# Kernel optimization log

Measured on AMD Instinct MI355X. Metric: run time of the kernel, lower is better.

## Reference

```python
import jax, jax.numpy as jnp
import numpy as np

BN_EPS = 1e-5


def setup_inputs() -> dict:
    key = jax.random.key(0)
    k1, k2, k3 = jax.random.split(key, 3)
    N, C_in, T, V = 32, 64, 288, 25
    C_out = 64
    fv = jax.random.normal(k1, (N, C_in, T, V), dtype=jnp.float32)
    adj = jax.random.uniform(k2, (V, V), dtype=jnp.float32)
    # Conv2d(2*C_in, C_out, 1x1) weight flattened to [C_out, 2*C_in]; kaiming-ish scale
    W = jax.random.normal(k3, (C_out, 2 * C_in), dtype=jnp.float32) * (2.0 / (2 * C_in)) ** 0.5
    b = jnp.zeros((C_out,), dtype=jnp.float32)
    gamma = jnp.ones((C_out,), dtype=jnp.float32)   # bn_init scale=1
    beta = jnp.zeros((C_out,), dtype=jnp.float32)
    return {"fv": fv, "adj": adj, "W": W, "b": b, "gamma": gamma, "beta": beta}


def reference(fv, adj, W, b, gamma, beta):
    # fv: [N, C, T, V]; neighbor aggregation over joints via learnable adjacency
    fv_agg = jnp.einsum('nctv,vy->ncty', fv, adj)
    cat = jnp.concatenate([fv, fv_agg], axis=1)            # [N, 2C, T, V]
    # 1x1 conv == channel matmul
    out = jnp.einsum('ncty,oc->noty', cat, W) + b[None, :, None, None]
    # BatchNorm2d in training mode: batch stats over (N, T, V) per channel
    mean = out.mean(axis=(0, 2, 3), keepdims=True)
    var = out.var(axis=(0, 2, 3), keepdims=True)
    out = (out - mean) * jax.lax.rsqrt(var + BN_EPS)
    out = out * gamma[None, :, None, None] + beta[None, :, None, None]
    return jax.nn.relu(out)
```

## Files before the change

### kernel.cpp

```cpp
#include <hip/hip_runtime.h>

#define N_DIM 32
#define C_IN 64
#define C_OUT 64
#define T_DIM 288
#define V_DIM 25
#define TV 7200
#define NTV 230400
#define TOTAL 14745600
#define BN_EPS 1e-5f

#define WS_WT1 0
#define WS_WT2 4096
#define WS_SUM 8192
#define WS_SQ  8256

__global__ __launch_bounds__(256) void prep_kernel(const float* __restrict__ W,
                                                   float* __restrict__ ws) {
  const int tid = threadIdx.x;
  if (tid < 128) ws[WS_SUM + tid] = 0.0f;
  for (int i = tid; i < 4096; i += 256) {
    const int c = i >> 6;
    const int o = i & 63;
    ws[WS_WT1 + i] = W[o * 128 + c];
    ws[WS_WT2 + i] = W[o * 128 + 64 + c];
  }
}

__device__ __forceinline__ float reduce32_lane(float* v, int lane) {
#pragma unroll
  for (int s = 0; s < 5; ++s) {
    const int m = 1 << s;
    const bool up = (lane & m) != 0;
    const int pairs = 32 >> (s + 1);
#pragma unroll
    for (int q = 0; q < pairs; ++q) {
      const float keep = up ? v[2 * q + 1] : v[2 * q];
      const float send = up ? v[2 * q] : v[2 * q + 1];
      const float recv = __shfl_xor(send, m, 64);
      v[q] = keep + recv;
    }
  }
  return v[0];
}

__global__ __launch_bounds__(64) void main_kernel(const float* __restrict__ fv,
                                                  const float* __restrict__ adj,
                                                  float* __restrict__ ws,
                                                  float* __restrict__ out) {
  const int j = blockIdx.x * 64 + threadIdx.x;
  const int n = j / TV;
  const int r = j - n * TV;
  const int t = r / V_DIM;
  const int y = r - t * V_DIM;
  const int lane = threadIdx.x & 63;

  float adjcol[V_DIM];
#pragma unroll
  for (int v = 0; v < V_DIM; ++v) adjcol[v] = adj[v * V_DIM + y];

  const float* __restrict__ wt1 = ws + WS_WT1;
  const float* __restrict__ wt2 = ws + WS_WT2;
  const float* base = fv + (size_t)n * (C_IN * TV) + t * V_DIM;

  float acc[C_OUT];
#pragma unroll
  for (int o = 0; o < C_OUT; ++o) acc[o] = 0.0f;

  for (int c = 0; c < C_IN; ++c) {
    const float* p = base + c * TV;
    const float x = p[y];
    float xa0 = 0.f, xa1 = 0.f, xa2 = 0.f, xa3 = 0.f;
#pragma unroll
    for (int v = 0; v < 24; v += 4) {
      xa0 = fmaf(p[v + 0], adjcol[v + 0], xa0);
      xa1 = fmaf(p[v + 1], adjcol[v + 1], xa1);
      xa2 = fmaf(p[v + 2], adjcol[v + 2], xa2);
      xa3 = fmaf(p[v + 3], adjcol[v + 3], xa3);
    }
    xa0 = fmaf(p[24], adjcol[24], xa0);
    const float xa = (xa0 + xa1) + (xa2 + xa3);

    const float* __restrict__ w1 = wt1 + c * 64;
    const float* __restrict__ w2 = wt2 + c * 64;
#pragma unroll
    for (int o = 0; o < C_OUT; ++o)
      acc[o] = fmaf(x, w1[o], fmaf(xa, w2[o], acc[o]));
  }

  float* op = out + (size_t)n * (C_OUT * TV) + t * V_DIM + y;
#pragma unroll
  for (int o = 0; o < C_OUT; ++o) op[o * TV] = acc[o];

  float* gsum = ws + WS_SUM;
  float* gsq = ws + WS_SQ;

  float sq[32];
#pragma unroll
  for (int i = 0; i < 32; ++i) sq[i] = acc[i] * acc[i];
  float s0 = reduce32_lane(acc, lane);
  s0 += __shfl_xor(s0, 32, 64);
  float q0 = reduce32_lane(sq, lane);
  q0 += __shfl_xor(q0, 32, 64);

#pragma unroll
  for (int i = 0; i < 32; ++i) sq[i] = acc[32 + i] * acc[32 + i];
  float s1 = reduce32_lane(acc + 32, lane);
  s1 += __shfl_xor(s1, 32, 64);
  float q1 = reduce32_lane(sq, lane);
  q1 += __shfl_xor(q1, 32, 64);

  if (lane < 32) {
    atomicAdd(&gsum[lane], s0);
    atomicAdd(&gsum[32 + lane], s1);
    atomicAdd(&gsq[lane], q0);
    atomicAdd(&gsq[32 + lane], q1);
  }
}

__global__ __launch_bounds__(256) void bn_kernel(const float* __restrict__ ws,
                                                 const float* __restrict__ gamma,
                                                 const float* __restrict__ beta,
                                                 float* __restrict__ out) {
  __shared__ float s_scale[C_OUT];
  __shared__ float s_shift[C_OUT];
  const int tid = threadIdx.x;
  if (tid < C_OUT) {
    const float inv = 1.0f / (float)NTV;
    const float mean = ws[WS_SUM + tid] * inv;
    const float var = fmaf(ws[WS_SQ + tid], inv, -mean * mean);
    const float sc = gamma[tid] * rsqrtf(var + BN_EPS);
    s_scale[tid] = sc;
    s_shift[tid] = fmaf(-mean, sc, beta[tid]);
  }
  __syncthreads();

  float4* o4 = reinterpret_cast<float4*>(out);
  const int total4 = TOTAL / 4;
  const int stride = gridDim.x * blockDim.x;
  for (int i = blockIdx.x * blockDim.x + tid; i < total4; i += stride) {
    float4 v = o4[i];
    const int o = (i / 1800) & 63;
    const float sc = s_scale[o];
    const float sh = s_shift[o];
    v.x = fmaxf(fmaf(v.x, sc, sh), 0.0f);
    v.y = fmaxf(fmaf(v.y, sc, sh), 0.0f);
    v.z = fmaxf(fmaf(v.z, sc, sh), 0.0f);
    v.w = fmaxf(fmaf(v.w, sc, sh), 0.0f);
    o4[i] = v;
  }
}

extern "C" void kernel_launch(void* const* d_in, const int* in_sizes, int n_in,
                              void* d_out, int out_size, void* d_ws, size_t ws_size,
                              hipStream_t stream) {
  const float* fv = (const float*)d_in[0];
  const float* adj = (const float*)d_in[1];
  const float* W = (const float*)d_in[2];
  const float* gamma = (const float*)d_in[4];
  const float* beta = (const float*)d_in[5];
  float* out = (float*)d_out;
  float* ws = (float*)d_ws;

  hipLaunchKernelGGL(prep_kernel, dim3(1), dim3(256), 0, stream, W, ws);
  hipLaunchKernelGGL(main_kernel, dim3(NTV / 64), dim3(64), 0, stream,
                     fv, adj, ws, out);
  hipLaunchKernelGGL(bn_kernel, dim3(2048), dim3(256), 0, stream,
                     ws, gamma, beta, out);
}
```

Measured before the change: 281.0 us.

## Split output channels across two thread halves and aggregate BN stats in LDS

Each block now has 256 threads covering 128 columns, and each thread computes 32 of the 64 output channels instead of all 64. Accumulator registers are halved, which should raise occupancy, and the weights are interleaved so the W1 and W2 values for a channel sit next to each other. Per-warp stat partials are first combined in shared memory, so each block issues only 128 global atomics, cutting global atomic traffic. In exchange, the adjacency aggregation and fv loads are done twice, once per thread half.

```diff
diff --git a/kernel.cpp b/kernel.cpp
--- a/kernel.cpp
+++ b/kernel.cpp
@@ -10,8 +10,7 @@
 #define TOTAL 14745600
 #define BN_EPS 1e-5f
 
-#define WS_WT1 0
-#define WS_WT2 4096
+#define WS_WINT 0
 #define WS_SUM 8192
 #define WS_SQ  8256
 
@@ -19,11 +18,13 @@
                                                    float* __restrict__ ws) {
   const int tid = threadIdx.x;
   if (tid < 128) ws[WS_SUM + tid] = 0.0f;
-  for (int i = tid; i < 4096; i += 256) {
-    const int c = i >> 6;
-    const int o = i & 63;
-    ws[WS_WT1 + i] = W[o * 128 + c];
-    ws[WS_WT2 + i] = W[o * 128 + 64 + c];
+  for (int i = tid; i < 8192; i += 256) {
+    const int s = i & 1;
+    const int oo = (i >> 1) & 31;
+    const int half = (i >> 6) & 1;
+    const int c = i >> 7;
+    const int o = half * 32 + oo;
+    ws[WS_WINT + i] = W[o * 128 + s * 64 + c];
   }
 }
 
@@ -44,28 +45,37 @@
   return v[0];
 }
 
-__global__ __launch_bounds__(64) void main_kernel(const float* __restrict__ fv,
-                                                  const float* __restrict__ adj,
-                                                  float* __restrict__ ws,
-                                                  float* __restrict__ out) {
-  const int j = blockIdx.x * 64 + threadIdx.x;
-  const int n = j / TV;
-  const int r = j - n * TV;
+__global__ __launch_bounds__(256) void main_kernel(const float* __restrict__ fv,
+                                                   const float* __restrict__ adj,
+                                                   const float* __restrict__ wint,
+                                                   float* __restrict__ stats,
+                                                   float* __restrict__ out) {
+  __shared__ float lsum[C_OUT];
+  __shared__ float lsq[C_OUT];
+  const int tid = threadIdx.x;
+  if (tid < 64) lsum[tid] = 0.0f;
+  else if (tid < 128) lsq[tid - 64] = 0.0f;
+  __syncthreads();
+
+  const int half = tid >> 7;
+  const int col = (blockIdx.x << 7) + (tid & 127);
+  const int lane = tid & 63;
+
+  const int n = col / TV;
+  const int r = col - n * TV;
   const int t = r / V_DIM;
   const int y = r - t * V_DIM;
-  const int lane = threadIdx.x & 63;
 
   float adjcol[V_DIM];
 #pragma unroll
   for (int v = 0; v < V_DIM; ++v) adjcol[v] = adj[v * V_DIM + y];
 
-  const float* __restrict__ wt1 = ws + WS_WT1;
-  const float* __restrict__ wt2 = ws + WS_WT2;
   const float* base = fv + (size_t)n * (C_IN * TV) + t * V_DIM;
+  const float* wbase = wint + half * 64;
 
-  float acc[C_OUT];
+  float acc[32];
 #pragma unroll
-  for (int o = 0; o < C_OUT; ++o) acc[o] = 0.0f;
+  for (int oo = 0; oo < 32; ++oo) acc[oo] = 0.0f;
 
   for (int c = 0; c < C_IN; ++c) {
     const float* p = base + c * TV;
@@ -81,44 +91,37 @@
     xa0 = fmaf(p[24], adjcol[24], xa0);
     const float xa = (xa0 + xa1) + (xa2 + xa3);
 
-    const float* __restrict__ w1 = wt1 + c * 64;
-    const float* __restrict__ w2 = wt2 + c * 64;
+    const float* __restrict__ w = wbase + c * 128;
 #pragma unroll
-    for (int o = 0; o < C_OUT; ++o)
-      acc[o] = fmaf(x, w1[o], fmaf(xa, w2[o], acc[o]));
+    for (int oo = 0; oo < 32; ++oo)
+      acc[oo] = fmaf(x, w[oo * 2], fmaf(xa, w[oo * 2 + 1], acc[oo]));
   }
 
-  float* op = out + (size_t)n * (C_OUT * TV) + t * V_DIM + y;
+  float* op = out + (size_t)n * (C_OUT * TV) + (size_t)(half * 32) * TV
+              + t * V_DIM + y;
 #pragma unroll
-  for (int o = 0; o < C_OUT; ++o) op[o * TV] = acc[o];
-
-  float* gsum = ws + WS_SUM;
-  float* gsq = ws + WS_SQ;
+  for (int oo = 0; oo < 32; ++oo) op[oo * TV] = acc[oo];
 
   float sq[32];
 #pragma unroll
   for (int i = 0; i < 32; ++i) sq[i] = acc[i] * acc[i];
-  float s0 = reduce32_lane(acc, lane);
-  s0 += __shfl_xor(s0, 32, 64);
-  float q0 = reduce32_lane(sq, lane);
-  q0 += __shfl_xor(q0, 32, 64);
-
-#pragma unroll
-  for (int i = 0; i < 32; ++i) sq[i] = acc[32 + i] * acc[32 + i];
-  float s1 = reduce32_lane(acc + 32, lane);
-  s1 += __shfl_xor(s1, 32, 64);
-  float q1 = reduce32_lane(sq, lane);
-  q1 += __shfl_xor(q1, 32, 64);
+  float s = reduce32_lane(acc, lane);
+  s += __shfl_xor(s, 32, 64);
+  float q = reduce32_lane(sq, lane);
+  q += __shfl_xor(q, 32, 64);
 
   if (lane < 32) {
-    atomicAdd(&gsum[lane], s0);
-    atomicAdd(&gsum[32 + lane], s1);
-    atomicAdd(&gsq[lane], q0);
-    atomicAdd(&gsq[32 + lane], q1);
+    atomicAdd(&lsum[half * 32 + lane], s);
+    atomicAdd(&lsq[half * 32 + lane], q);
+  }
+  __syncthreads();
+  if (tid < 64) {
+    atomicAdd(&stats[tid], lsum[tid]);
+    atomicAdd(&stats[64 + tid], lsq[tid]);
   }
 }
 
-__global__ __launch_bounds__(256) void bn_kernel(const float* __restrict__ ws,
+__global__ __launch_bounds__(256) void bn_kernel(const float* __restrict__ stats,
                                                  const float* __restrict__ gamma,
                                                  const float* __restrict__ beta,
                                                  float* __restrict__ out) {
@@ -127,8 +130,8 @@
   const int tid = threadIdx.x;
   if (tid < C_OUT) {
     const float inv = 1.0f / (float)NTV;
-    const float mean = ws[WS_SUM + tid] * inv;
-    const float var = fmaf(ws[WS_SQ + tid], inv, -mean * mean);
+    const float mean = stats[tid] * inv;
+    const float var = fmaf(stats[64 + tid], inv, -mean * mean);
     const float sc = gamma[tid] * rsqrtf(var + BN_EPS);
     s_scale[tid] = sc;
     s_shift[tid] = fmaf(-mean, sc, beta[tid]);
@@ -163,8 +166,8 @@
   float* ws = (float*)d_ws;
 
   hipLaunchKernelGGL(prep_kernel, dim3(1), dim3(256), 0, stream, W, ws);
-  hipLaunchKernelGGL(main_kernel, dim3(NTV / 64), dim3(64), 0, stream,
-                     fv, adj, ws, out);
+  hipLaunchKernelGGL(main_kernel, dim3(NTV / 128), dim3(256), 0, stream,
+                     fv, adj, ws + WS_WINT, ws + WS_SUM, out);
   hipLaunchKernelGGL(bn_kernel, dim3(2048), dim3(256), 0, stream,
-                     ws, gamma, beta, out);
+                     ws + WS_SUM, gamma, beta, out);
 }
```

Result: slower. 547.5 us (+94.9%).
